# Kernel optimization log

Measured on AMD Instinct MI355X. Metric: run time of the kernel, lower is better.

## Reference

```python
import jax, jax.numpy as jnp
import numpy as np

N = 4096
M = 1024
APPERTURE = 250
L1, L2, L3, PRED = 1024, 512, 128, 1
EPS = 1e-6


def _layer_norm(x, gamma, beta):
    # torch x.std(-1) is unbiased (ddof=1)
    mean = jnp.mean(x, axis=-1, keepdims=True)
    std = jnp.std(x, axis=-1, ddof=1, keepdims=True)
    return gamma * (x - mean) / (std + EPS) + beta


def _self_attention(x, Wq, Wk, Wv, Wo, band_mask):
    # x: [n, m]; Linear(bias=False) => x @ W.T
    K = x @ Wk.T
    Q = (x @ Wq.T) * 0.06
    V = x @ Wv.T
    logits = Q @ K.T                      # [n, n]
    logits = jnp.where(band_mask, logits, -jnp.inf)  # keep |i-j| < apperture
    att = jax.nn.softmax(logits, axis=-1)
    # original: y = (V^T @ att)^T == att^T @ V  (note the transpose!)
    y = att.T @ V
    return y @ Wo.T, att


def setup_inputs() -> dict:
    key = jax.random.key(0)
    ks = jax.random.split(key, 20)
    s = 0.02
    inp = {
        'x1': jax.random.normal(ks[0], (1, N, M), jnp.float32),
        'x2': jax.random.normal(ks[1], (1, N, M), jnp.float32),
        'x3': jax.random.normal(ks[2], (1, N, M), jnp.float32),
        'Wq': jax.random.normal(ks[3], (M, M), jnp.float32) * s,
        'Wk': jax.random.normal(ks[4], (M, M), jnp.float32) * s,
        'Wv': jax.random.normal(ks[5], (M, M), jnp.float32) * s,
        'Wo': jax.random.normal(ks[6], (M, M), jnp.float32) * s,
        'ka_w': jax.random.normal(ks[7], (L1, M), jnp.float32) * s,
        'ka_b': jnp.zeros((L1,), jnp.float32),
        'kb_w': jax.random.normal(ks[8], (L2, L1), jnp.float32) * s,
        'kb_b': jnp.zeros((L2,), jnp.float32),
        'kc_w': jax.random.normal(ks[9], (L3, L2), jnp.float32) * s,
        'kc_b': jnp.zeros((L3,), jnp.float32),
        'kd_w': jax.random.normal(ks[10], (PRED, L3), jnp.float32) * s,
        'kd_b': jnp.zeros((PRED,), jnp.float32),
        'g13': jnp.ones((M,), jnp.float32),
        'b13': jnp.zeros((M,), jnp.float32),
        'gkc': jnp.ones((L3,), jnp.float32),
        'bkc': jnp.zeros((L3,), jnp.float32),
        'seq_len': N,
    }
    return inp


def reference(x1, x2, x3, Wq, Wk, Wv, Wo, ka_w, ka_b, kb_w, kb_b, kc_w, kc_b,
              kd_w, kd_b, g13, b13, gkc, bkc, seq_len):
    x1 = x1.reshape(-1, x1.shape[2])
    x2 = x2.reshape(-1, x2.shape[2])
    x3 = x3.reshape(-1, x3.shape[2])
    n = x1.shape[0]
    idx = jnp.arange(n)
    band_mask = jnp.abs(idx[:, None] - idx[None, :]) < APPERTURE  # allowed

    y1, att1 = _self_attention(x1, Wq, Wk, Wv, Wo, band_mask)
    y2, _ = _self_attention(x2, Wq, Wk, Wv, Wo, band_mask)
    y3, _ = _self_attention(x3, Wq, Wk, Wv, Wo, band_mask)

    # residual + (dropout == identity in eval) + shared LayerNorm
    y1 = _layer_norm(y1 + x1, g13, b13)
    y2 = _layer_norm(y2 + x2, g13, b13)
    y3 = _layer_norm(y3 + x3, g13, b13)

    y = y1 + y2 + y3  # cmb == [1,1,1]
    y = y @ ka_w.T + ka_b
    y = y @ kb_w.T + kb_b
    y = jax.nn.relu(y @ kc_w.T + kc_b)
    y = _layer_norm(y, gkc, bkc)
    y = jax.nn.sigmoid(y @ kd_w.T + kd_b)
    return y.reshape(1, -1), att1
```

## Files before the change

kernel.cpp:

```cpp
#include <hip/hip_runtime.h>
#include <hip/hip_bf16.h>
#include <cstdint>
#include <cstddef>

#define NSEQ 4096
#define MDIM 1024

typedef __attribute__((ext_vector_type(8))) short short8;
typedef __attribute__((ext_vector_type(4))) float f32x4;
typedef __attribute__((ext_vector_type(2))) long long2v;
typedef __attribute__((ext_vector_type(8))) int int8v;
typedef __attribute__((ext_vector_type(4))) int int4v;

typedef const __attribute__((address_space(1))) void gvoid_t;
typedef __attribute__((address_space(3))) void lvoid_t;

__device__ __forceinline__ unsigned short f2b(float x) {
  union { float f; unsigned int u; } a; a.f = x;
  unsigned int r = (a.u + 0x7fffu + ((a.u >> 16) & 1u)) >> 16;
  return (unsigned short)r;
}
__device__ __forceinline__ float b2f(unsigned short u) {
  union { float f; unsigned int u32; } a; a.u32 = ((unsigned int)u) << 16;
  return a.f;
}
__device__ __forceinline__ unsigned char f2e4(float x) {
  return (unsigned char)(__builtin_amdgcn_cvt_pk_fp8_f32(x, x, 0, false) & 0xff);
}
__device__ __forceinline__ unsigned int f2e4x4(float a, float b, float c, float d) {
  unsigned int lo = __builtin_amdgcn_cvt_pk_fp8_f32(a, b, 0, false);
  return (unsigned int)__builtin_amdgcn_cvt_pk_fp8_f32(c, d, lo, true);
}

__device__ __forceinline__ int8v pack32(const unsigned char* p0,
                                        const unsigned char* p1) {
  int4v lo = *(const int4v*)p0;
  int4v hi = *(const int4v*)p1;
  int8v r;
  r[0] = lo[0]; r[1] = lo[1]; r[2] = lo[2]; r[3] = lo[3];
  r[4] = hi[0]; r[5] = hi[1]; r[6] = hi[2]; r[7] = hi[3];
  return r;
}

__global__ __launch_bounds__(256) void k_cvt_all(
    const float* __restrict__ s0, const float* __restrict__ s1,
    const float* __restrict__ s2, const float* __restrict__ s3,
    const float* __restrict__ s4, const float* __restrict__ s5,
    const float* __restrict__ s6,
    const float* __restrict__ xa, const float* __restrict__ xb,
    const float* __restrict__ xc,
    unsigned char* __restrict__ Wf8, unsigned short* __restrict__ Wmlp,
    unsigned char* __restrict__ Xdst) {
  int idx = blockIdx.x * 256 + threadIdx.x;
  if (idx < 1048576) {
    int seg = idx >> 18, local = idx & 262143;
    const float* src = (seg == 0) ? s0 : (seg == 1) ? s1 : (seg == 2) ? s2 : s3;
    float4 v = *(const float4*)(src + (size_t)local * 4);
    *(unsigned int*)(Wf8 + (size_t)idx * 4) =
        f2e4x4(v.x * 64.f, v.y * 64.f, v.z * 64.f, v.w * 64.f);
  } else if (idx < 1458176) {
    int i2 = idx - 1048576;
    const float* src; int local;
    if (i2 < 262144) { src = s4; local = i2; }
    else if (i2 < 393216) { src = s5; local = i2 - 262144; }
    else { src = s6; local = i2 - 393216; }
    float4 v = *(const float4*)(src + (size_t)local * 4);
    ushort4 o; o.x = f2b(v.x); o.y = f2b(v.y); o.z = f2b(v.z); o.w = f2b(v.w);
    *(ushort4*)(Wmlp + (size_t)i2 * 4) = o;
  } else {
    int i2 = idx - 1458176;
    int seg = i2 >> 20, local = i2 & 1048575;
    const float* src = (seg == 0) ? xa : (seg == 1) ? xb : xc;
    float4 v = *(const float4*)(src + (size_t)local * 4);
    *(unsigned int*)(Xdst + (size_t)i2 * 4) = f2e4x4(v.x, v.y, v.z, v.w);
  }
}

__global__ __launch_bounds__(256) void k_gemm(
    const unsigned char* __restrict__ A, int lda,
    const unsigned char* __restrict__ B, int ldb,
    void* __restrict__ Cout, void* __restrict__ Cout2, int ldc,
    int K, float alpha, int okind, int do_exp, int mode,
    const unsigned char* __restrict__ A1, const unsigned char* __restrict__ A2) {
  __shared__ unsigned char smem[2 * 128 * 128];
  unsigned char* As = smem;
  unsigned char* Bs = smem + 128 * 128;
  int bx = blockIdx.x, by = blockIdx.y;
  const unsigned char* Ab;
  const unsigned char* Bb;
  void* Cdst = Cout;
  int k0 = 0, k1 = K, b_koff = 0;
  int ldce = ldc;
  int rbase, cbase;
  int ldae = lda, ldbe = ldb;
  if (mode == 0) {
    Ab = A + (size_t)by * 128 * lda;
    Bb = B + (size_t)bx * 128 * ldb;
    rbase = bx * 128; cbase = by * 128;
  } else if (mode == 3) {
    if (by < 16) {
      Ab = A + (size_t)by * 128 * lda;
      Bb = B + (size_t)bx * 128 * ldb;
      if (by >= 8) Cdst = Cout2;
      rbase = bx * 128; cbase = (by & 7) * 128;
    } else {
      Ab = B + (size_t)bx * 128 * ldb;
      Bb = A1 + (size_t)(by - 16) * 128 * 1024;
      Cdst = (void*)const_cast<unsigned char*>(A2);
      rbase = (by - 16) * 128; cbase = bx * 128;
      ldce = 3 * NSEQ;
    }
  } else if (mode == 1) {
    int s = bx >> 5, ti = bx & 31;
    int bt = ti + by - 2;
    if (bt < 0 || bt >= 32) return;
    Ab = A + (size_t)(s * 32 + bt) * 128 * lda;
    Bb = B + (size_t)bx * 128 * ldb;
    rbase = bx * 128; cbase = by * 128;
  } else {
    int s = bx >> 5, ti = bx & 31;
    Ab = A + (size_t)by * 128 * lda + s * NSEQ;
    const unsigned char* Bbase = (s == 0) ? B : ((s == 1) ? A1 : A2);
    Bb = Bbase + (size_t)ti * 128 * 640;
    ldbe = 640;
    int lo = ti - 2; if (lo < 0) lo = 0;
    int hi = ti + 3; if (hi > 32) hi = 32;
    k0 = lo * 128; k1 = hi * 128;
    b_koff = (ti - 2) * 128;
    rbase = bx * 128; cbase = by * 128;
  }

  const int t = threadIdx.x;
  const int l = t & 63;
  const int w = t >> 6;
  const int fr = l & 15;
  const int quad = l >> 4;
  const int wm = (w >> 1) * 64;
  const int wn = (w & 1) * 64;
  const int fq4 = quad * 4;

  int srow[4], scg[4], sloff[4];
#pragma unroll
  for (int j = 0; j < 4; j++) {
    srow[j] = w * 32 + j * 8 + (l >> 3);
    scg[j] = ((l & 7) - srow[j]) & 7;
    sloff[j] = (w * 32 + j * 8) * 128 + l * 16;
  }

  f32x4 acc[4][4];
#pragma unroll
  for (int m = 0; m < 4; m++)
#pragma unroll
    for (int n = 0; n < 4; n++) acc[m][n] = (f32x4){0.f, 0.f, 0.f, 0.f};

  const int c0 = quad * 2;
  for (int kk = k0; kk < k1; kk += 128) {
    int kb = kk - b_koff;
    __syncthreads();
#pragma unroll
    for (int j = 0; j < 4; j++)
      __builtin_amdgcn_global_load_lds(
          (gvoid_t*)(Ab + (size_t)srow[j] * ldae + kk + scg[j] * 16),
          (lvoid_t*)(As + sloff[j]), 16, 0, 0);
#pragma unroll
    for (int j = 0; j < 4; j++)
      __builtin_amdgcn_global_load_lds(
          (gvoid_t*)(Bb + (size_t)srow[j] * ldbe + kb + scg[j] * 16),
          (lvoid_t*)(Bs + sloff[j]), 16, 0, 0);
    __syncthreads();
    {
      int8v a8[4], b8[4];
#pragma unroll
      for (int m = 0; m < 4; m++) {
        int r = wm + m * 16 + fr;
        int s0i = (c0 + r) & 7, s1i = (s0i + 1) & 7;
        a8[m] = pack32(As + r * 128 + s0i * 16, As + r * 128 + s1i * 16);
      }
#pragma unroll
      for (int n = 0; n < 4; n++) {
        int r = wn + n * 16 + fr;
        int s0i = (c0 + r) & 7, s1i = (s0i + 1) & 7;
        b8[n] = pack32(Bs + r * 128 + s0i * 16, Bs + r * 128 + s1i * 16);
      }
#pragma unroll
      for (int m = 0; m < 4; m++)
#pragma unroll
        for (int n = 0; n < 4; n++)
          acc[m][n] = __builtin_amdgcn_mfma_scale_f32_16x16x128_f8f6f4(
              a8[m], b8[n], acc[m][n], 0, 0, 0, 0x7F7F7F7F, 0, 0x7F7F7F7F);
    }
  }

#pragma unroll
  for (int m = 0; m < 4; m++) {
#pragma unroll
    for (int n = 0; n < 4; n++) {
      int oc = cbase + wm + m * 16 + fq4;
      int orow = rbase + wn + n * 16 + fr;
      float v0 = acc[m][n][0] * alpha, v1 = acc[m][n][1] * alpha;
      float v2 = acc[m][n][2] * alpha, v3 = acc[m][n][3] * alpha;
      if (okind == 1) {
        if (do_exp) { v0 = __expf(v0); v1 = __expf(v1); v2 = __expf(v2); v3 = __expf(v3); }
        ushort4 o; o.x = f2b(v0); o.y = f2b(v1); o.z = f2b(v2); o.w = f2b(v3);
        *(uint2*)((unsigned short*)Cdst + (size_t)orow * ldce + oc) = *(uint2*)&o;
      } else if (okind == 2) {
        *(unsigned int*)((unsigned char*)Cdst + (size_t)orow * ldce + oc) =
            f2e4x4(v0, v1, v2, v3);
      } else {
        *(float4*)((float*)Cdst + (size_t)orow * ldce + oc) = make_float4(v0, v1, v2, v3);
      }
    }
  }
}

__global__ __launch_bounds__(256) void k_gemm64(
    const unsigned short* __restrict__ A, int lda,
    const unsigned short* __restrict__ B, int ldb,
    void* __restrict__ Cout, int ldc, int K,
    const float* __restrict__ bias, int relu, int out_bf16) {
  __shared__ unsigned short smem[2 * 64 * 64];
  unsigned short* As = smem;
  unsigned short* Bs = smem + 64 * 64;
  int bx = blockIdx.x, by = blockIdx.y;
  const unsigned short* Ab = A + (size_t)by * 64 * lda;
  const unsigned short* Bb = B + (size_t)bx * 64 * ldb;
  int rbase = bx * 64, cbase = by * 64;

  const int t = threadIdx.x;
  const int l = t & 63;
  const int w = t >> 6;
  const int fr = l & 15;
  const int quad = l >> 4;
  const int wm = (w & 1) * 32;
  const int wn = (w >> 1) * 32;
  const int fq4 = quad * 4;

  int srow[2], scg[2], sloff[2];
#pragma unroll
  for (int j = 0; j < 2; j++) {
    srow[j] = w * 16 + j * 8 + (l >> 3);
    scg[j] = ((l & 7) - srow[j]) & 7;
    sloff[j] = (w * 16 + j * 8) * 64 + l * 8;
  }

  f32x4 acc[2][2];
#pragma unroll
  for (int m = 0; m < 2; m++)
#pragma unroll
    for (int n = 0; n < 2; n++) acc[m][n] = (f32x4){0.f, 0.f, 0.f, 0.f};

  for (int kk = 0; kk < K; kk += 64) {
    __syncthreads();
#pragma unroll
    for (int j = 0; j < 2; j++)
      __builtin_amdgcn_global_load_lds(
          (gvoid_t*)(Ab + (size_t)srow[j] * lda + kk + scg[j] * 8),
          (lvoid_t*)(As + sloff[j]), 16, 0, 0);
#pragma unroll
    for (int j = 0; j < 2; j++)
      __builtin_amdgcn_global_load_lds(
          (gvoid_t*)(Bb + (size_t)srow[j] * ldb + kk + scg[j] * 8),
          (lvoid_t*)(Bs + sloff[j]), 16, 0, 0);
    __syncthreads();
#pragma unroll
    for (int s = 0; s < 2; s++) {
      short8 af[2], bf[2];
#pragma unroll
      for (int m = 0; m < 2; m++) {
        int r = wm + m * 16 + fr;
        int slot = (s * 4 + quad + r) & 7;
        af[m] = *(const short8*)(As + r * 64 + slot * 8);
      }
#pragma unroll
      for (int n = 0; n < 2; n++) {
        int r = wn + n * 16 + fr;
        int slot = (s * 4 + quad + r) & 7;
        bf[n] = *(const short8*)(Bs + r * 64 + slot * 8);
      }
#pragma unroll
      for (int m = 0; m < 2; m++)
#pragma unroll
        for (int n = 0; n < 2; n++)
          acc[m][n] = __builtin_amdgcn_mfma_f32_16x16x32_bf16(af[m], bf[n], acc[m][n], 0, 0, 0);
    }
  }

#pragma unroll
  for (int m = 0; m < 2; m++) {
#pragma unroll
    for (int n = 0; n < 2; n++) {
      int oc = cbase + wm + m * 16 + fq4;
      int orow = rbase + wn + n * 16 + fr;
      float4 bv = bias ? *(const float4*)(bias + oc) : make_float4(0.f, 0.f, 0.f, 0.f);
      float v0 = acc[m][n][0] + bv.x, v1 = acc[m][n][1] + bv.y;
      float v2 = acc[m][n][2] + bv.z, v3 = acc[m][n][3] + bv.w;
      if (relu) {
        v0 = fmaxf(v0, 0.f); v1 = fmaxf(v1, 0.f);
        v2 = fmaxf(v2, 0.f); v3 = fmaxf(v3, 0.f);
      }
      if (out_bf16) {
        ushort4 o; o.x = f2b(v0); o.y = f2b(v1); o.z = f2b(v2); o.w = f2b(v3);
        *(uint2*)((unsigned short*)Cout + (size_t)orow * ldc + oc) = *(uint2*)&o;
      } else {
        *(float4*)((float*)Cout + (size_t)orow * ldc + oc) = make_float4(v0, v1, v2, v3);
      }
    }
  }
}

__global__ __launch_bounds__(256) void k_stats(const unsigned short* __restrict__ Eband,
                                               float* __restrict__ sums) {
  int ig = blockIdx.x * 4 + (threadIdx.x >> 6);
  int lane = threadIdx.x & 63;
  int i = ig & 4095;
  int ti = i >> 7;
  int cbase = (ti - 2) * 128;
  int jlo = i - 249; if (jlo < 0) jlo = 0;
  int jhi = i + 249; if (jhi > NSEQ - 1) jhi = NSEQ - 1;
  int clo = jlo - cbase, chi = jhi - cbase;
  const unsigned short* L = Eband + (size_t)ig * 640;
  float s = 0.f;
  for (int c = clo + lane; c <= chi; c += 64) s += b2f(L[c]);
  for (int off = 32; off; off >>= 1) s += __shfl_xor(s, off);
  if (lane == 0) sums[ig] = s;
}

__global__ __launch_bounds__(256) void k_build_attT(const unsigned short* __restrict__ Eband,
                                                    const float* __restrict__ sums,
                                                    unsigned char* __restrict__ t0,
                                                    unsigned char* __restrict__ t1,
                                                    unsigned char* __restrict__ t2) {
  int byy = blockIdx.y;
  int s = byy >> 5, ti = byy & 31;
  int tj = ti + (int)blockIdx.x - 2;
  if (tj < 0 || tj >= 32) return;
  unsigned char* dst = (s == 0) ? t0 : ((s == 1) ? t1 : t2);
  __shared__ unsigned char T[128][132];
  int t = threadIdx.x;
  int c0 = (ti - tj + 2) * 128;
  int colg = (t & 31) * 4;
  for (int jj = t >> 5; jj < 128; jj += 8) {
    int jg = s * NSEQ + tj * 128 + jj;
    float inv = 16.f / sums[jg];
    ushort4 v = *(const ushort4*)&Eband[(size_t)jg * 640 + c0 + colg];
    float vv[4] = {b2f(v.x), b2f(v.y), b2f(v.z), b2f(v.w)};
#pragma unroll
    for (int q = 0; q < 4; q++) {
      int i = ti * 128 + colg + q;
      int d = i - (tj * 128 + jj);
      float a = (d < 250 && d > -250) ? vv[q] * inv : 0.f;
      T[colg + q][jj] = f2e4(a);
    }
  }
  __syncthreads();
  int jb0 = (tj - ti + 2) * 128;
  for (int ii = t >> 5; ii < 128; ii += 8) {
    size_t o = (size_t)(ti * 128 + ii) * 640 + jb0 + colg;
    *(unsigned int*)(dst + o) = *(const unsigned int*)&T[ii][colg];
  }
}

__global__ __launch_bounds__(256) void k_write_att(const unsigned short* __restrict__ Eband,
                                                   const float* __restrict__ sums,
                                                   float* __restrict__ att) {
  int i = blockIdx.x;
  int ti = i >> 7, cbase = (ti - 2) * 128;
  int jlo = i - 249; if (jlo < 0) jlo = 0;
  int jhi = i + 249; if (jhi > NSEQ - 1) jhi = NSEQ - 1;
  float inv = 1.f / sums[i];
  const unsigned short* L = Eband + (size_t)i * 640;
  float* arow = att + (size_t)i * NSEQ;
  for (int j0 = threadIdx.x * 4; j0 < NSEQ; j0 += 1024) {
    float ov[4];
#pragma unroll
    for (int q = 0; q < 4; q++) {
      int j = j0 + q;
      ov[q] = (j >= jlo && j <= jhi) ? b2f(L[j - cbase]) * inv : 0.f;
    }
    *(float4*)(arow + j0) = make_float4(ov[0], ov[1], ov[2], ov[3]);
  }
}

__global__ __launch_bounds__(256) void k_ln3(const unsigned short* __restrict__ yo,
                                             const float* __restrict__ x1,
                                             const float* __restrict__ x2,
                                             const float* __restrict__ x3,
                                             const float* __restrict__ g,
                                             const float* __restrict__ b,
                                             unsigned short* __restrict__ ysum_b) {
  int i = blockIdx.x, t = threadIdx.x;
  int w = t >> 6, lane = t & 63;
  __shared__ float red[8];
  const float* xs[3] = {x1, x2, x3};
  float4 gg = *(const float4*)(g + t * 4);
  float4 bb = *(const float4*)(b + t * 4);
  float acc[4] = {0.f, 0.f, 0.f, 0.f};
  for (int s = 0; s < 3; s++) {
    ushort4 yv = *(const ushort4*)(yo + ((size_t)(s * NSEQ + i)) * MDIM + t * 4);
    float4 xx = *(const float4*)(xs[s] + (size_t)i * MDIM + t * 4);
    float v[4] = {b2f(yv.x) + xx.x, b2f(yv.y) + xx.y, b2f(yv.z) + xx.z, b2f(yv.w) + xx.w};
    float s1 = v[0] + v[1] + v[2] + v[3];
    float s2 = v[0]*v[0] + v[1]*v[1] + v[2]*v[2] + v[3]*v[3];
    for (int off = 32; off; off >>= 1) { s1 += __shfl_xor(s1, off); s2 += __shfl_xor(s2, off); }
    __syncthreads();
    if (lane == 0) { red[w] = s1; red[4 + w] = s2; }
    __syncthreads();
    float S1 = red[0] + red[1] + red[2] + red[3];
    float S2 = red[4] + red[5] + red[6] + red[7];
    float mean = S1 * (1.f / 1024.f);
    float var = (S2 - S1 * mean) * (1.f / 1023.f);
    float rstd = 1.f / (sqrtf(var) + 1e-6f);
    acc[0] += gg.x * (v[0] - mean) * rstd + bb.x;
    acc[1] += gg.y * (v[1] - mean) * rstd + bb.y;
    acc[2] += gg.z * (v[2] - mean) * rstd + bb.z;
    acc[3] += gg.w * (v[3] - mean) * rstd + bb.w;
  }
  ushort4 o;
  o.x = f2b(acc[0]); o.y = f2b(acc[1]); o.z = f2b(acc[2]); o.w = f2b(acc[3]);
  *(ushort4*)(ysum_b + (size_t)i * MDIM + t * 4) = o;
}

__global__ __launch_bounds__(128) void k_final(const float* __restrict__ h3,
                                               const float* __restrict__ g,
                                               const float* __restrict__ b,
                                               const float* __restrict__ kdw,
                                               const float* __restrict__ kdb,
                                               float* __restrict__ yout) {
  int i = blockIdx.x, t = threadIdx.x;
  float v = h3[(size_t)i * 128 + t];
  float s1 = v, s2 = v * v;
  for (int off = 32; off; off >>= 1) { s1 += __shfl_xor(s1, off); s2 += __shfl_xor(s2, off); }
  __shared__ float red[4];
  int w = t >> 6, lane = t & 63;
  if (lane == 0) { red[w] = s1; red[2 + w] = s2; }
  __syncthreads();
  float S1 = red[0] + red[1], S2 = red[2] + red[3];
  float mean = S1 * (1.f / 128.f);
  float var = (S2 - S1 * mean) * (1.f / 127.f);
  float rstd = 1.f / (sqrtf(var) + 1e-6f);
  float ln = g[t] * (v - mean) * rstd + b[t];
  float p = ln * kdw[t];
  for (int off = 32; off; off >>= 1) p += __shfl_xor(p, off);
  __syncthreads();
  if (lane == 0) red[w] = p;
  __syncthreads();
  if (t == 0) {
    float z = red[0] + red[1] + kdb[0];
    yout[i] = 1.f / (1.f + __expf(-z));
  }
}

extern "C" void kernel_launch(void* const* d_in, const int* in_sizes, int n_in,
                              void* d_out, int out_size, void* d_ws, size_t ws_size,
                              hipStream_t stream) {
  const float* x1 = (const float*)d_in[0];
  const float* x2 = (const float*)d_in[1];
  const float* x3 = (const float*)d_in[2];
  const float* Wq = (const float*)d_in[3];
  const float* Wk = (const float*)d_in[4];
  const float* Wv = (const float*)d_in[5];
  const float* Wo = (const float*)d_in[6];
  const float* ka_w = (const float*)d_in[7];
  const float* ka_b = (const float*)d_in[8];
  const float* kb_w = (const float*)d_in[9];
  const float* kb_b = (const float*)d_in[10];
  const float* kc_w = (const float*)d_in[11];
  const float* kc_b = (const float*)d_in[12];
  const float* kd_w = (const float*)d_in[13];
  const float* kd_b = (const float*)d_in[14];
  const float* g13 = (const float*)d_in[15];
  const float* b13 = (const float*)d_in[16];
  const float* gkc = (const float*)d_in[17];
  const float* bkc = (const float*)d_in[18];

  float* y_out = (float*)d_out;
  float* att_out = y_out + NSEQ;

  char* ws = (char*)d_ws;
  size_t off = 0;
  auto alloc = [&](size_t bytes) -> void* {
    void* p = ws + off;
    off += (bytes + 255) & ~(size_t)255;
    return p;
  };
  const size_t NM = (size_t)3 * NSEQ * MDIM;
  unsigned char* Wf = (unsigned char*)alloc(4 * 1048576);
  unsigned short* Wmlp = (unsigned short*)alloc((1048576 + 524288 + 65536) * 2);
  unsigned char* Xf = (unsigned char*)alloc(NM);
  unsigned char* Qf = (unsigned char*)alloc(NM);
  unsigned char* Kf = (unsigned char*)alloc(NM);
  unsigned char* VTf = (unsigned char*)alloc(NM);
  unsigned short* Eband = (unsigned short*)alloc((size_t)3 * NSEQ * 640 * 2);
  float* sums = (float*)alloc((size_t)3 * NSEQ * 4);
  unsigned char* aT0 = (unsigned char*)alloc((size_t)NSEQ * 640);
  unsigned char* aT1 = (unsigned char*)alloc((size_t)NSEQ * 640);
  unsigned char* aT2 = (unsigned char*)alloc((size_t)NSEQ * 640);
  unsigned char* Wv_f = Wf + 2097152;
  unsigned char* Wo_f = Wf + 3145728;
  unsigned short* ka_b16 = Wmlp;
  unsigned short* kb_b16 = Wmlp + 1048576;
  unsigned short* kc_b16 = Wmlp + 1572864;
  unsigned char* yb = Xf;
  unsigned short* yo = (unsigned short*)Qf;
  unsigned short* ysum_b = (unsigned short*)VTf;
  unsigned short* h1b = (unsigned short*)Xf;
  unsigned short* h2b = (unsigned short*)Qf;
  float* h3 = (float*)aT0;

  k_cvt_all<<<17984, 256, 0, stream>>>(Wq, Wk, Wv, Wo, ka_w, kb_w, kc_w,
                                       x1, x2, x3, Wf, Wmlp, Xf);

  k_gemm<<<dim3(96, 24), 256, 0, stream>>>(Wf, 1024, Xf, 1024, Qf, Kf, 1024,
                                           1024, 1.f / 64.f, 2, 0, 3, Wv_f, VTf);
  k_gemm<<<dim3(96, 5), 256, 0, stream>>>(Kf, 1024, Qf, 1024, Eband, nullptr, 640,
                                          1024, 0.06f, 1, 1, 1, nullptr, nullptr);
  k_stats<<<3072, 256, 0, stream>>>(Eband, sums);
  k_build_attT<<<dim3(5, 96), 256, 0, stream>>>(Eband, sums, aT0, aT1, aT2);
  k_gemm<<<dim3(96, 8), 256, 0, stream>>>(VTf, 3 * NSEQ, aT0, 640, yb, nullptr, 1024,
                                          NSEQ, 0.5f, 2, 0, 2, aT1, aT2);
  k_write_att<<<4096, 256, 0, stream>>>(Eband, sums, att_out);
  k_gemm<<<dim3(96, 8), 256, 0, stream>>>(Wo_f, 1024, yb, 1024, yo, nullptr, 1024,
                                          1024, 1.f / 512.f, 1, 0, 0, nullptr, nullptr);
  k_ln3<<<4096, 256, 0, stream>>>(yo, x1, x2, x3, g13, b13, ysum_b);

  k_gemm64<<<dim3(64, 16), 256, 0, stream>>>(ka_b16, 1024, ysum_b, 1024, h1b, 1024,
                                             1024, ka_b, 0, 1);
  k_gemm64<<<dim3(64, 8), 256, 0, stream>>>(kb_b16, 1024, h1b, 1024, h2b, 512,
                                            1024, kb_b, 0, 1);
  k_gemm64<<<dim3(64, 2), 256, 0, stream>>>(kc_b16, 512, h2b, 512, h3, 128,
                                            512, kc_b, 1, 0);
  k_final<<<4096, 128, 0, stream>>>(h3, gkc, bkc, kd_w, kd_b, y_out);
}
```

Measured before the change: 343.4 us.

## Double-buffer LDS tiles in FP8 and BF16 GEMM kernels

Both GEMM kernels now use two LDS buffers. The next K-tile's global_load_lds is issued before the current tile's MFMA work, and there is one barrier per iteration instead of two. The aim is to hide global-memory latency behind the matrix math and cut synchronisation. In exchange, LDS per block doubles (64 KB for the FP8 kernel), which can lower occupancy, and correctness relies on the barrier waiting for the async LDS loads to finish.

Result: no change. 339.8 us (-1.0%).

```diff
diff --git a/kernel.cpp b/kernel.cpp
--- a/kernel.cpp
+++ b/kernel.cpp
@@ -82,9 +82,7 @@
     void* __restrict__ Cout, void* __restrict__ Cout2, int ldc,
     int K, float alpha, int okind, int do_exp, int mode,
     const unsigned char* __restrict__ A1, const unsigned char* __restrict__ A2) {
-  __shared__ unsigned char smem[2 * 128 * 128];
-  unsigned char* As = smem;
-  unsigned char* Bs = smem + 128 * 128;
+  __shared__ unsigned char smem[4 * 128 * 128];
   int bx = blockIdx.x, by = blockIdx.y;
   const unsigned char* Ab;
   const unsigned char* Bb;
@@ -154,41 +152,59 @@
     for (int n = 0; n < 4; n++) acc[m][n] = (f32x4){0.f, 0.f, 0.f, 0.f};
 
   const int c0 = quad * 2;
-  for (int kk = k0; kk < k1; kk += 128) {
-    int kb = kk - b_koff;
-    __syncthreads();
+  const int nt = (k1 - k0) >> 7;
+
+  {
+    int kk = k0, kb = kk - b_koff;
 #pragma unroll
     for (int j = 0; j < 4; j++)
       __builtin_amdgcn_global_load_lds(
           (gvoid_t*)(Ab + (size_t)srow[j] * ldae + kk + scg[j] * 16),
-          (lvoid_t*)(As + sloff[j]), 16, 0, 0);
+          (lvoid_t*)(smem + sloff[j]), 16, 0, 0);
 #pragma unroll
     for (int j = 0; j < 4; j++)
       __builtin_amdgcn_global_load_lds(
           (gvoid_t*)(Bb + (size_t)srow[j] * ldbe + kb + scg[j] * 16),
-          (lvoid_t*)(Bs + sloff[j]), 16, 0, 0);
+          (lvoid_t*)(smem + 16384 + sloff[j]), 16, 0, 0);
+  }
+
+  for (int tt = 0; tt < nt; tt++) {
     __syncthreads();
-    {
-      int8v a8[4], b8[4];
-#pragma unroll
-      for (int m = 0; m < 4; m++) {
-        int r = wm + m * 16 + fr;
-        int s0i = (c0 + r) & 7, s1i = (s0i + 1) & 7;
-        a8[m] = pack32(As + r * 128 + s0i * 16, As + r * 128 + s1i * 16);
-      }
-#pragma unroll
-      for (int n = 0; n < 4; n++) {
-        int r = wn + n * 16 + fr;
-        int s0i = (c0 + r) & 7, s1i = (s0i + 1) & 7;
-        b8[n] = pack32(Bs + r * 128 + s0i * 16, Bs + r * 128 + s1i * 16);
-      }
-#pragma unroll
-      for (int m = 0; m < 4; m++)
-#pragma unroll
-        for (int n = 0; n < 4; n++)
-          acc[m][n] = __builtin_amdgcn_mfma_scale_f32_16x16x128_f8f6f4(
-              a8[m], b8[n], acc[m][n], 0, 0, 0, 0x7F7F7F7F, 0, 0x7F7F7F7F);
-    }
+    if (tt + 1 < nt) {
+      int kk = k0 + (tt + 1) * 128, kb = kk - b_koff;
+      unsigned char* Asn = smem + ((tt + 1) & 1) * 32768;
+#pragma unroll
+      for (int j = 0; j < 4; j++)
+        __builtin_amdgcn_global_load_lds(
+            (gvoid_t*)(Ab + (size_t)srow[j] * ldae + kk + scg[j] * 16),
+            (lvoid_t*)(Asn + sloff[j]), 16, 0, 0);
+#pragma unroll
+      for (int j = 0; j < 4; j++)
+        __builtin_amdgcn_global_load_lds(
+            (gvoid_t*)(Bb + (size_t)srow[j] * ldbe + kb + scg[j] * 16),
+            (lvoid_t*)(Asn + 16384 + sloff[j]), 16, 0, 0);
+    }
+    const unsigned char* Asc = smem + (tt & 1) * 32768;
+    const unsigned char* Bsc = Asc + 16384;
+    int8v a8[4], b8[4];
+#pragma unroll
+    for (int m = 0; m < 4; m++) {
+      int r = wm + m * 16 + fr;
+      int s0i = (c0 + r) & 7, s1i = (s0i + 1) & 7;
+      a8[m] = pack32(Asc + r * 128 + s0i * 16, Asc + r * 128 + s1i * 16);
+    }
+#pragma unroll
+    for (int n = 0; n < 4; n++) {
+      int r = wn + n * 16 + fr;
+      int s0i = (c0 + r) & 7, s1i = (s0i + 1) & 7;
+      b8[n] = pack32(Bsc + r * 128 + s0i * 16, Bsc + r * 128 + s1i * 16);
+    }
+#pragma unroll
+    for (int m = 0; m < 4; m++)
+#pragma unroll
+      for (int n = 0; n < 4; n++)
+        acc[m][n] = __builtin_amdgcn_mfma_scale_f32_16x16x128_f8f6f4(
+            a8[m], b8[n], acc[m][n], 0, 0, 0, 0x7F7F7F7F, 0, 0x7F7F7F7F);
   }
 
 #pragma unroll
@@ -218,9 +234,7 @@
     const unsigned short* __restrict__ B, int ldb,
     void* __restrict__ Cout, int ldc, int K,
     const float* __restrict__ bias, int relu, int out_bf16) {
-  __shared__ unsigned short smem[2 * 64 * 64];
-  unsigned short* As = smem;
-  unsigned short* Bs = smem + 64 * 64;
+  __shared__ unsigned short smem[4 * 64 * 64];
   int bx = blockIdx.x, by = blockIdx.y;
   const unsigned short* Ab = A + (size_t)by * 64 * lda;
   const unsigned short* Bb = B + (size_t)bx * 64 * ldb;
@@ -249,19 +263,37 @@
 #pragma unroll
     for (int n = 0; n < 2; n++) acc[m][n] = (f32x4){0.f, 0.f, 0.f, 0.f};
 
-  for (int kk = 0; kk < K; kk += 64) {
+  const int nt = K >> 6;
+
+#pragma unroll
+  for (int j = 0; j < 2; j++)
+    __builtin_amdgcn_global_load_lds(
+        (gvoid_t*)(Ab + (size_t)srow[j] * lda + scg[j] * 8),
+        (lvoid_t*)(smem + sloff[j]), 16, 0, 0);
+#pragma unroll
+  for (int j = 0; j < 2; j++)
+    __builtin_amdgcn_global_load_lds(
+        (gvoid_t*)(Bb + (size_t)srow[j] * ldb + scg[j] * 8),
+        (lvoid_t*)(smem + 4096 + sloff[j]), 16, 0, 0);
+
+  for (int tt = 0; tt < nt; tt++) {
     __syncthreads();
-#pragma unroll
-    for (int j = 0; j < 2; j++)
-      __builtin_amdgcn_global_load_lds(
-          (gvoid_t*)(Ab + (size_t)srow[j] * lda + kk + scg[j] * 8),
-          (lvoid_t*)(As + sloff[j]), 16, 0, 0);
-#pragma unroll
-    for (int j = 0; j < 2; j++)
-      __builtin_amdgcn_global_load_lds(
-          (gvoid_t*)(Bb + (size_t)srow[j] * ldb + kk + scg[j] * 8),
-          (lvoid_t*)(Bs + sloff[j]), 16, 0, 0);
-    __syncthreads();
+    if (tt + 1 < nt) {
+      int kk = (tt + 1) * 64;
+      unsigned short* Asn = smem + ((tt + 1) & 1) * 8192;
+#pragma unroll
+      for (int j = 0; j < 2; j++)
+        __builtin_amdgcn_global_load_lds(
+            (gvoid_t*)(Ab + (size_t)srow[j] * lda + kk + scg[j] * 8),
+            (lvoid_t*)(Asn + sloff[j]), 16, 0, 0);
+#pragma unroll
+      for (int j = 0; j < 2; j++)
+        __builtin_amdgcn_global_load_lds(
+            (gvoid_t*)(Bb + (size_t)srow[j] * ldb + kk + scg[j] * 8),
+            (lvoid_t*)(Asn + 4096 + sloff[j]), 16, 0, 0);
+    }
+    const unsigned short* Asc = smem + (tt & 1) * 8192;
+    const unsigned short* Bsc = Asc + 4096;
 #pragma unroll
     for (int s = 0; s < 2; s++) {
       short8 af[2], bf[2];
@@ -269,13 +301,13 @@
       for (int m = 0; m < 2; m++) {
         int r = wm + m * 16 + fr;
         int slot = (s * 4 + quad + r) & 7;
-        af[m] = *(const short8*)(As + r * 64 + slot * 8);
+        af[m] = *(const short8*)(Asc + r * 64 + slot * 8);
       }
 #pragma unroll
       for (int n = 0; n < 2; n++) {
         int r = wn + n * 16 + fr;
         int slot = (s * 4 + quad + r) & 7;
-        bf[n] = *(const short8*)(Bs + r * 64 + slot * 8);
+        bf[n] = *(const short8*)(Bsc + r * 64 + slot * 8);
       }
 #pragma unroll
       for (int m = 0; m < 2; m++)
```
